# Performance work log

Measured on AMD Instinct MI355X. Metric: run time of the kernel, lower is better.

The kernel has to match this reference:

```python
import jax, jax.numpy as jnp
import numpy as np

N_NODES = 100000
N_EDGES = 1600000
N_FEAT = 512
N_HID = 256
N_CLASS = 40


def setup_inputs() -> dict:
    key = jax.random.key(0)
    ks = jax.random.split(key, 6)
    features = jax.random.normal(ks[0], (N_NODES, N_FEAT), dtype=jnp.float32)
    edge_index = jax.random.randint(ks[1], (2, N_EDGES), 0, N_NODES, dtype=jnp.int32)
    edge_weight = jax.random.uniform(ks[2], (N_EDGES,), dtype=jnp.float32)
    # xavier_uniform with gain=1.414 (as in reset_parameters)
    g = 1.414
    lim1 = g * np.sqrt(6.0 / (N_FEAT + N_HID))
    lim2 = g * np.sqrt(6.0 / (N_HID + N_CLASS))
    W1 = jax.random.uniform(ks[3], (N_FEAT, N_HID), minval=-lim1, maxval=lim1, dtype=jnp.float32)
    W2 = jax.random.uniform(ks[4], (N_HID, N_CLASS), minval=-lim2, maxval=lim2, dtype=jnp.float32)
    b1 = jnp.zeros((N_HID,), dtype=jnp.float32)
    b2 = jnp.zeros((N_CLASS,), dtype=jnp.float32)
    return {"features": features, "edge_index": edge_index, "edge_weight": edge_weight,
            "W1": W1, "b1": b1, "W2": W2, "b2": b2}


def _spmm(edge_index, edge_weight, x, n):
    # out[r] = sum over edges e with row[e]==r of w[e] * x[col[e]]
    row, col = edge_index[0], edge_index[1]
    msgs = edge_weight[:, None] * x[col]  # [E, D]
    return jax.ops.segment_sum(msgs, row, num_segments=n)


def reference(features, edge_index, edge_weight, W1, b1, W2, b2):
    n = features.shape[0]
    # Layer 1: linear -> spmm -> relu (dropout is identity in eval mode)
    h = features @ W1 + b1
    h = jax.nn.relu(_spmm(edge_index, edge_weight, h, n))
    # Layer 2: linear -> spmm -> log_softmax
    h = h @ W2 + b2
    h = _spmm(edge_index, edge_weight, h, n)
    return jax.nn.log_softmax(h, axis=1)
```

## Files before the change

kernel.cpp:

```cpp
#include <hip/hip_runtime.h>
#include <stdint.h>

#define N_NODES 100000
#define N_EDGES 1600000
#define N_FEAT 512
#define N_HID 256
#define N_CLASS 40
#define H2S 48

typedef float f32x4 __attribute__((ext_vector_type(4)));
typedef __bf16 bf16x8 __attribute__((ext_vector_type(8)));
typedef unsigned short u16x4 __attribute__((ext_vector_type(4)));
typedef unsigned short u16x8 __attribute__((ext_vector_type(8)));

__device__ __forceinline__ unsigned short f2bf(float f) {
  unsigned int u = __float_as_uint(f);
  unsigned int r = (u + 0x7FFFu + ((u >> 16) & 1u)) >> 16;
  return (unsigned short)r;
}
__device__ __forceinline__ float bf2f(unsigned short s) {
  return __uint_as_float(((unsigned int)s) << 16);
}

#define HIST_BLOCKS 1563
#define W1T_BLOCKS  512
#define W2T_BLOCKS  48
__global__ __launch_bounds__(256) void k_pre(const float* __restrict__ W1,
                                             const float* __restrict__ W2,
                                             const int* __restrict__ ei,
                                             unsigned short* __restrict__ W1t,
                                             unsigned short* __restrict__ W2t,
                                             int* __restrict__ cnt,
                                             int* __restrict__ rank) {
  const int bid = blockIdx.x, tid = threadIdx.x;
  if (bid < HIST_BLOCKS) {
    #pragma unroll
    for (int k = 0; k < 4; ++k) {
      int e = bid * 1024 + k * 256 + tid;
      if (e < N_EDGES) rank[e] = atomicAdd(&cnt[ei[e]], 1);
    }
  } else if (bid < HIST_BLOCKS + W1T_BLOCKS) {
    int gid = (bid - HIST_BLOCKS) * 256 + tid;
    int n = gid >> 9, k = gid & 511;
    W1t[gid] = f2bf(W1[(long)k * N_HID + n]);
  } else {
    int gid = (bid - HIST_BLOCKS - W1T_BLOCKS) * 256 + tid;
    int n = gid >> 8, k = gid & 255;
    W2t[gid] = (n < N_CLASS) ? f2bf(W2[(long)k * N_CLASS + n]) : (unsigned short)0;
  }
}

__global__ __launch_bounds__(1024) void k_scan_a(const int* __restrict__ cnt,
                                                 int* __restrict__ rp,
                                                 int* __restrict__ bsum) {
  __shared__ int sm[1024];
  const int tid = threadIdx.x;
  const int i = blockIdx.x * 1024 + tid;
  int v = (i < N_NODES) ? cnt[i] : 0;
  sm[tid] = v;
  __syncthreads();
  #pragma unroll
  for (int d = 1; d < 1024; d <<= 1) {
    int t = (tid >= d) ? sm[tid - d] : 0;
    __syncthreads();
    sm[tid] += t;
    __syncthreads();
  }
  if (i < N_NODES) rp[i] = sm[tid] - v;
  if (tid == 1023) bsum[blockIdx.x] = sm[1023];
}

__global__ __launch_bounds__(128) void k_scan_b(const int* __restrict__ bsum,
                                                int* __restrict__ boffs,
                                                int* __restrict__ rp) {
  __shared__ int sm[128];
  const int tid = threadIdx.x;
  const int nb = (N_NODES + 1023) >> 10;
  int v = (tid < nb) ? bsum[tid] : 0;
  sm[tid] = v;
  __syncthreads();
  #pragma unroll
  for (int d = 1; d < 128; d <<= 1) {
    int t = (tid >= d) ? sm[tid - d] : 0;
    __syncthreads();
    sm[tid] += t;
    __syncthreads();
  }
  boffs[tid] = sm[tid] - v;
  if (tid == 127) rp[N_NODES] = sm[127];
}

__global__ void k_scan_c(int* __restrict__ rp, const int* __restrict__ boffs) {
  int i = blockIdx.x * 256 + threadIdx.x;
  if (i >= N_NODES) return;
  rp[i] += boffs[i >> 10];
}

#define NG1 782
__global__ __launch_bounds__(512) void k_fused1(const float* __restrict__ X,
                                                const unsigned short* __restrict__ W1t,
                                                const float* __restrict__ b1,
                                                unsigned short* __restrict__ H1,
                                                const int* __restrict__ ei,
                                                const float* __restrict__ ew,
                                                const int* __restrict__ rank,
                                                const int* __restrict__ rp,
                                                int2* __restrict__ cw) {
  __shared__ unsigned short As[128][40];
  __shared__ unsigned short Bs[256][40];
  const int t = threadIdx.x;

  if (blockIdx.x & 1) {
    int sb = blockIdx.x >> 1;
    #pragma unroll
    for (int k = 0; k < 4; ++k) {
      int e = sb * 2048 + k * 512 + t;
      if (e < N_EDGES) {
        int r = ei[e];
        int pos = rp[r] + rank[e];
        cw[pos] = make_int2(ei[N_EDGES + e], __float_as_int(ew[e]));
      }
    }
    return;
  }

  const int gb = blockIdx.x >> 1;
  const int lane = t & 63;
  const int wid = t >> 6;
  const int wm = wid >> 2, wn = wid & 3;
  const long m0 = (long)gb * 128;

  f32x4 acc[4][4] = {};
  const int ar = t >> 2;
  const int ak = (t & 3) * 8;
  const long arow = m0 + ar;
  const bool avalid = arow < N_NODES;
  const float* xs = X + arow * N_FEAT;
  const unsigned short* ws0 = W1t + (long)ar * N_FEAT;
  const unsigned short* ws1 = W1t + (long)(ar + 128) * N_FEAT;

  f32x4 xa = {}, xb = {};
  if (avalid) { xa = *(const f32x4*)(xs + ak); xb = *(const f32x4*)(xs + ak + 4); }
  u16x8 wa = *(const u16x8*)(ws0 + ak);
  u16x8 wb = *(const u16x8*)(ws1 + ak);

  for (int k0 = 0; k0 < N_FEAT; k0 += 32) {
    __syncthreads();
    u16x8 ap;
    ap[0] = f2bf(xa[0]); ap[1] = f2bf(xa[1]); ap[2] = f2bf(xa[2]); ap[3] = f2bf(xa[3]);
    ap[4] = f2bf(xb[0]); ap[5] = f2bf(xb[1]); ap[6] = f2bf(xb[2]); ap[7] = f2bf(xb[3]);
    *(u16x8*)&As[ar][ak] = ap;
    *(u16x8*)&Bs[ar][ak] = wa;
    *(u16x8*)&Bs[ar + 128][ak] = wb;
    __syncthreads();

    if (k0 + 32 < N_FEAT) {
      int ko = k0 + 32 + ak;
      if (avalid) { xa = *(const f32x4*)(xs + ko); xb = *(const f32x4*)(xs + ko + 4); }
      wa = *(const u16x8*)(ws0 + ko);
      wb = *(const u16x8*)(ws1 + ko);
    }

    bf16x8 a[4], b[4];
    #pragma unroll
    for (int mt = 0; mt < 4; ++mt)
      a[mt] = *(const bf16x8*)&As[wm * 64 + mt * 16 + (lane & 15)][(lane >> 4) * 8];
    #pragma unroll
    for (int nt = 0; nt < 4; ++nt)
      b[nt] = *(const bf16x8*)&Bs[wn * 64 + nt * 16 + (lane & 15)][(lane >> 4) * 8];
    #pragma unroll
    for (int mt = 0; mt < 4; ++mt)
      #pragma unroll
      for (int nt = 0; nt < 4; ++nt)
        acc[mt][nt] = __builtin_amdgcn_mfma_f32_16x16x32_bf16(a[mt], b[nt], acc[mt][nt], 0, 0, 0);
  }

  #pragma unroll
  for (int nt = 0; nt < 4; ++nt) {
    int col = wn * 64 + nt * 16 + (lane & 15);
    float bias = b1[col];
    #pragma unroll
    for (int mt = 0; mt < 4; ++mt) {
      #pragma unroll
      for (int i = 0; i < 4; ++i) {
        long row = m0 + wm * 64 + mt * 16 + (lane >> 4) * 4 + i;
        if (row < N_NODES) H1[row * N_HID + col] = f2bf(acc[mt][nt][i] + bias);
      }
    }
  }
}

__global__ __launch_bounds__(256) void k_spmm1(const int* __restrict__ row_ptr,
                                               const int2* __restrict__ cw,
                                               const unsigned short* __restrict__ H1,
                                               unsigned short* __restrict__ H1r) {
  int r = blockIdx.x * 4 + (threadIdx.x >> 6);
  int lane = threadIdx.x & 63;
  if (r >= N_NODES) return;
  int s = row_ptr[r], e = row_ptr[r + 1];
  float a0 = 0.f, a1 = 0.f, a2 = 0.f, a3 = 0.f;
  const unsigned short* Hb = H1 + lane * 4;
  int i = s;
  for (; i + 8 <= e; i += 8) {
    int2 c0 = cw[i + 0]; int2 c1 = cw[i + 1]; int2 c2 = cw[i + 2]; int2 c3 = cw[i + 3];
    int2 c4 = cw[i + 4]; int2 c5 = cw[i + 5]; int2 c6 = cw[i + 6]; int2 c7 = cw[i + 7];
    u16x4 h0 = *(const u16x4*)(Hb + (long)c0.x * N_HID);
    u16x4 h1 = *(const u16x4*)(Hb + (long)c1.x * N_HID);
    u16x4 h2 = *(const u16x4*)(Hb + (long)c2.x * N_HID);
    u16x4 h3 = *(const u16x4*)(Hb + (long)c3.x * N_HID);
    u16x4 h4 = *(const u16x4*)(Hb + (long)c4.x * N_HID);
    u16x4 h5 = *(const u16x4*)(Hb + (long)c5.x * N_HID);
    u16x4 h6 = *(const u16x4*)(Hb + (long)c6.x * N_HID);
    u16x4 h7 = *(const u16x4*)(Hb + (long)c7.x * N_HID);
    float w0 = __int_as_float(c0.y), w1 = __int_as_float(c1.y);
    float w2 = __int_as_float(c2.y), w3 = __int_as_float(c3.y);
    float w4 = __int_as_float(c4.y), w5 = __int_as_float(c5.y);
    float w6 = __int_as_float(c6.y), w7 = __int_as_float(c7.y);
    a0 += w0 * bf2f(h0[0]); a1 += w0 * bf2f(h0[1]); a2 += w0 * bf2f(h0[2]); a3 += w0 * bf2f(h0[3]);
    a0 += w1 * bf2f(h1[0]); a1 += w1 * bf2f(h1[1]); a2 += w1 * bf2f(h1[2]); a3 += w1 * bf2f(h1[3]);
    a0 += w2 * bf2f(h2[0]); a1 += w2 * bf2f(h2[1]); a2 += w2 * bf2f(h2[2]); a3 += w2 * bf2f(h2[3]);
    a0 += w3 * bf2f(h3[0]); a1 += w3 * bf2f(h3[1]); a2 += w3 * bf2f(h3[2]); a3 += w3 * bf2f(h3[3]);
    a0 += w4 * bf2f(h4[0]); a1 += w4 * bf2f(h4[1]); a2 += w4 * bf2f(h4[2]); a3 += w4 * bf2f(h4[3]);
    a0 += w5 * bf2f(h5[0]); a1 += w5 * bf2f(h5[1]); a2 += w5 * bf2f(h5[2]); a3 += w5 * bf2f(h5[3]);
    a0 += w6 * bf2f(h6[0]); a1 += w6 * bf2f(h6[1]); a2 += w6 * bf2f(h6[2]); a3 += w6 * bf2f(h6[3]);
    a0 += w7 * bf2f(h7[0]); a1 += w7 * bf2f(h7[1]); a2 += w7 * bf2f(h7[2]); a3 += w7 * bf2f(h7[3]);
  }
  for (; i < e; ++i) {
    int2 cwv = cw[i];
    float w = __int_as_float(cwv.y);
    u16x4 hv = *(const u16x4*)(Hb + (long)cwv.x * N_HID);
    a0 += w * bf2f(hv[0]);
    a1 += w * bf2f(hv[1]);
    a2 += w * bf2f(hv[2]);
    a3 += w * bf2f(hv[3]);
  }
  u16x4 o;
  o[0] = f2bf(fmaxf(a0, 0.f));
  o[1] = f2bf(fmaxf(a1, 0.f));
  o[2] = f2bf(fmaxf(a2, 0.f));
  o[3] = f2bf(fmaxf(a3, 0.f));
  *(u16x4*)(H1r + (long)r * N_HID + lane * 4) = o;
}

__global__ __launch_bounds__(256) void k_gemm2(const unsigned short* __restrict__ H1r,
                                               const unsigned short* __restrict__ W2t,
                                               const float* __restrict__ b2,
                                               float* __restrict__ H2) {
  __shared__ unsigned short As[128][40];
  __shared__ unsigned short Bs[48][40];
  const int t = threadIdx.x;
  const int lane = t & 63;
  const int wid = t >> 6;
  const long m0 = (long)blockIdx.x * 128;
  f32x4 acc[2][3] = {};

  for (int k0 = 0; k0 < N_HID; k0 += 32) {
    __syncthreads();
    #pragma unroll
    for (int p = 0; p < 2; ++p) {
      int u = t + p * 256;
      int rr = u >> 2, kk = (u & 3) * 8;
      long gr = m0 + rr;
      u16x8 v = {};
      if (gr < N_NODES) v = *(const u16x8*)(H1r + gr * N_HID + k0 + kk);
      *(u16x8*)&As[rr][kk] = v;
    }
    if (t < 192) {
      int rr = t >> 2, kk = (t & 3) * 8;
      *(u16x8*)&Bs[rr][kk] = *(const u16x8*)(W2t + (long)rr * N_HID + k0 + kk);
    }
    __syncthreads();

    bf16x8 a[2], b[3];
    #pragma unroll
    for (int mt = 0; mt < 2; ++mt)
      a[mt] = *(const bf16x8*)&As[wid * 32 + mt * 16 + (lane & 15)][(lane >> 4) * 8];
    #pragma unroll
    for (int nt = 0; nt < 3; ++nt)
      b[nt] = *(const bf16x8*)&Bs[nt * 16 + (lane & 15)][(lane >> 4) * 8];
    #pragma unroll
    for (int mt = 0; mt < 2; ++mt)
      #pragma unroll
      for (int nt = 0; nt < 3; ++nt)
        acc[mt][nt] = __builtin_amdgcn_mfma_f32_16x16x32_bf16(a[mt], b[nt], acc[mt][nt], 0, 0, 0);
  }

  #pragma unroll
  for (int nt = 0; nt < 3; ++nt) {
    int col = nt * 16 + (lane & 15);
    if (col < N_CLASS) {
      float bias = b2[col];
      #pragma unroll
      for (int mt = 0; mt < 2; ++mt) {
        #pragma unroll
        for (int i = 0; i < 4; ++i) {
          long row = m0 + wid * 32 + mt * 16 + (lane >> 4) * 4 + i;
          if (row < N_NODES) H2[row * H2S + col] = acc[mt][nt][i] + bias;
        }
      }
    }
  }
}

__global__ __launch_bounds__(256) void k_spmm2_lsm(const int* __restrict__ row_ptr,
                                                   const int2* __restrict__ cw,
                                                   const float* __restrict__ H2,
                                                   float* __restrict__ out) {
  int r = blockIdx.x * 4 + (threadIdx.x >> 6);
  int lane = threadIdx.x & 63;
  if (r >= N_NODES) return;
  int s = row_ptr[r], e = row_ptr[r + 1];
  float acc = 0.f;
  const bool act = lane < N_CLASS;
  int i = s;
  for (; i + 4 <= e; i += 4) {
    int2 c0 = cw[i + 0];
    int2 c1 = cw[i + 1];
    int2 c2 = cw[i + 2];
    int2 c3 = cw[i + 3];
    float h0 = 0.f, h1 = 0.f, h2 = 0.f, h3 = 0.f;
    if (act) {
      h0 = H2[(long)c0.x * H2S + lane];
      h1 = H2[(long)c1.x * H2S + lane];
      h2 = H2[(long)c2.x * H2S + lane];
      h3 = H2[(long)c3.x * H2S + lane];
    }
    acc += __int_as_float(c0.y) * h0;
    acc += __int_as_float(c1.y) * h1;
    acc += __int_as_float(c2.y) * h2;
    acc += __int_as_float(c3.y) * h3;
  }
  for (; i < e; ++i) {
    int2 cwv = cw[i];
    if (act) acc += __int_as_float(cwv.y) * H2[(long)cwv.x * H2S + lane];
  }
  float v = act ? acc : -INFINITY;
  float m = v;
  #pragma unroll
  for (int d = 32; d > 0; d >>= 1) m = fmaxf(m, __shfl_xor(m, d));
  float ex = act ? __expf(v - m) : 0.f;
  float ssum = ex;
  #pragma unroll
  for (int d = 32; d > 0; d >>= 1) ssum += __shfl_xor(ssum, d);
  float ls = __logf(ssum);
  if (act) out[(long)r * N_CLASS + lane] = v - m - ls;
}

extern "C" void kernel_launch(void* const* d_in, const int* in_sizes, int n_in,
                              void* d_out, int out_size, void* d_ws, size_t ws_size,
                              hipStream_t stream) {
  (void)in_sizes; (void)n_in; (void)out_size; (void)ws_size;
  const float* X  = (const float*)d_in[0];
  const int*   EI = (const int*)d_in[1];
  const float* EW = (const float*)d_in[2];
  const float* W1 = (const float*)d_in[3];
  const float* b1 = (const float*)d_in[4];
  const float* W2 = (const float*)d_in[5];
  const float* b2 = (const float*)d_in[6];
  float* out = (float*)d_out;

  char* p = (char*)d_ws;
  auto take = [&](size_t bytes) {
    char* r = p;
    p += (bytes + 511) & ~(size_t)511;
    return r;
  };
  unsigned short* W1t   = (unsigned short*)take((size_t)N_HID * N_FEAT * 2);
  unsigned short* W2t   = (unsigned short*)take((size_t)48 * N_HID * 2);
  int*            cnt   = (int*)take((size_t)N_NODES * 4);
  int*            rp    = (int*)take((size_t)(N_NODES + 1) * 4);
  int*            bsum  = (int*)take((size_t)128 * 4);
  int*            boffs = (int*)take((size_t)128 * 4);
  int*            rank  = (int*)take((size_t)N_EDGES * 4);
  int2*           cw    = (int2*)take((size_t)N_EDGES * 8);
  unsigned short* H1    = (unsigned short*)take((size_t)N_NODES * N_HID * 2);
  unsigned short* H1r   = (unsigned short*)take((size_t)N_NODES * N_HID * 2);
  float*          H2    = (float*)take((size_t)N_NODES * H2S * 4);

  const int NB_SCAN = (N_NODES + 1023) / 1024;

  hipMemsetAsync(cnt, 0, (size_t)N_NODES * 4, stream);
  k_pre<<<HIST_BLOCKS + W1T_BLOCKS + W2T_BLOCKS, 256, 0, stream>>>(W1, W2, EI, W1t, W2t, cnt, rank);
  k_scan_a<<<NB_SCAN, 1024, 0, stream>>>(cnt, rp, bsum);
  k_scan_b<<<1, 128, 0, stream>>>(bsum, boffs, rp);
  k_scan_c<<<(N_NODES + 255) / 256, 256, 0, stream>>>(rp, boffs);
  k_fused1<<<2 * NG1, 512, 0, stream>>>(X, W1t, b1, H1, EI, EW, rank, rp, cw);
  k_spmm1<<<(N_NODES + 3) / 4, 256, 0, stream>>>(rp, cw, H1, H1r);
  k_gemm2<<<(N_NODES + 127) / 128, 256, 0, stream>>>(H1r, W2t, b2, H2);
  k_spmm2_lsm<<<(N_NODES + 3) / 4, 256, 0, stream>>>(rp, cw, H2, out);
}
```

Measured before the change: 437.8 us.

## Load MFMA operands directly from global memory, dropping LDS staging in both GEMMs

Both GEMM kernels stop staging tiles through shared memory: each lane loads its MFMA fragments straight from global memory into registers, with a one-step register prefetch in the first GEMM, and all __syncthreads are removed. Out-of-range rows are clamped to the last valid row instead of being zero-filled. The spmm2 loop is also unrolled from 4 to 8 edges to keep more gathers in flight. The cost is that the global load traffic in GEMM1 is no longer shared across warps: each warp re-reads its own A and B fragments, so L2/global traffic and register pressure go up.

```diff
diff --git a/kernel.cpp b/kernel.cpp
--- a/kernel.cpp
+++ b/kernel.cpp
@@ -106,8 +106,6 @@
                                                 const int* __restrict__ rank,
                                                 const int* __restrict__ rp,
                                                 int2* __restrict__ cw) {
-  __shared__ unsigned short As[128][40];
-  __shared__ unsigned short Bs[256][40];
   const int t = threadIdx.x;
 
   if (blockIdx.x & 1) {
@@ -129,55 +127,68 @@
   const int wid = t >> 6;
   const int wm = wid >> 2, wn = wid & 3;
   const long m0 = (long)gb * 128;
+  const int lr = lane & 15;
+  const int lk = (lane >> 4) * 8;
+
+  const float* Ab[4];
+  #pragma unroll
+  for (int mt = 0; mt < 4; ++mt) {
+    long r = m0 + wm * 64 + mt * 16 + lr;
+    if (r >= N_NODES) r = N_NODES - 1;
+    Ab[mt] = X + r * N_FEAT + lk;
+  }
+  const unsigned short* Bb[4];
+  #pragma unroll
+  for (int nt = 0; nt < 4; ++nt)
+    Bb[nt] = W1t + (long)(wn * 64 + nt * 16 + lr) * N_FEAT + lk;
 
   f32x4 acc[4][4] = {};
-  const int ar = t >> 2;
-  const int ak = (t & 3) * 8;
-  const long arow = m0 + ar;
-  const bool avalid = arow < N_NODES;
-  const float* xs = X + arow * N_FEAT;
-  const unsigned short* ws0 = W1t + (long)ar * N_FEAT;
-  const unsigned short* ws1 = W1t + (long)(ar + 128) * N_FEAT;
-
-  f32x4 xa = {}, xb = {};
-  if (avalid) { xa = *(const f32x4*)(xs + ak); xb = *(const f32x4*)(xs + ak + 4); }
-  u16x8 wa = *(const u16x8*)(ws0 + ak);
-  u16x8 wb = *(const u16x8*)(ws1 + ak);
-
+  f32x4 xa[4], xb[4];
+  bf16x8 bv[4];
+  #pragma unroll
+  for (int mt = 0; mt < 4; ++mt) { xa[mt] = *(const f32x4*)(Ab[mt]); xb[mt] = *(const f32x4*)(Ab[mt] + 4); }
+  #pragma unroll
+  for (int nt = 0; nt < 4; ++nt) bv[nt] = *(const bf16x8*)(Bb[nt]);
+
+  #pragma unroll 2
   for (int k0 = 0; k0 < N_FEAT; k0 += 32) {
-    __syncthreads();
-    u16x8 ap;
-    ap[0] = f2bf(xa[0]); ap[1] = f2bf(xa[1]); ap[2] = f2bf(xa[2]); ap[3] = f2bf(xa[3]);
-    ap[4] = f2bf(xb[0]); ap[5] = f2bf(xb[1]); ap[6] = f2bf(xb[2]); ap[7] = f2bf(xb[3]);
-    *(u16x8*)&As[ar][ak] = ap;
-    *(u16x8*)&Bs[ar][ak] = wa;
-    *(u16x8*)&Bs[ar + 128][ak] = wb;
-    __syncthreads();
-
-    if (k0 + 32 < N_FEAT) {
-      int ko = k0 + 32 + ak;
-      if (avalid) { xa = *(const f32x4*)(xs + ko); xb = *(const f32x4*)(xs + ko + 4); }
-      wa = *(const u16x8*)(ws0 + ko);
-      wb = *(const u16x8*)(ws1 + ko);
-    }
-
-    bf16x8 a[4], b[4];
-    #pragma unroll
-    for (int mt = 0; mt < 4; ++mt)
-      a[mt] = *(const bf16x8*)&As[wm * 64 + mt * 16 + (lane & 15)][(lane >> 4) * 8];
-    #pragma unroll
-    for (int nt = 0; nt < 4; ++nt)
-      b[nt] = *(const bf16x8*)&Bs[wn * 64 + nt * 16 + (lane & 15)][(lane >> 4) * 8];
+    const int kn = (k0 + 32) & (N_FEAT - 1);
+    f32x4 nxa[4], nxb[4];
+    bf16x8 nbv[4];
+    #pragma unroll
+    for (int mt = 0; mt < 4; ++mt) {
+      nxa[mt] = *(const f32x4*)(Ab[mt] + kn);
+      nxb[mt] = *(const f32x4*)(Ab[mt] + kn + 4);
+    }
+    #pragma unroll
+    for (int nt = 0; nt < 4; ++nt) nbv[nt] = *(const bf16x8*)(Bb[nt] + kn);
+
+    bf16x8 av[4];
+    #pragma unroll
+    for (int mt = 0; mt < 4; ++mt) {
+      bf16x8 v;
+      v[0] = (__bf16)xa[mt][0]; v[1] = (__bf16)xa[mt][1];
+      v[2] = (__bf16)xa[mt][2]; v[3] = (__bf16)xa[mt][3];
+      v[4] = (__bf16)xb[mt][0]; v[5] = (__bf16)xb[mt][1];
+      v[6] = (__bf16)xb[mt][2]; v[7] = (__bf16)xb[mt][3];
+      av[mt] = v;
+    }
+
     #pragma unroll
     for (int mt = 0; mt < 4; ++mt)
       #pragma unroll
       for (int nt = 0; nt < 4; ++nt)
-        acc[mt][nt] = __builtin_amdgcn_mfma_f32_16x16x32_bf16(a[mt], b[nt], acc[mt][nt], 0, 0, 0);
+        acc[mt][nt] = __builtin_amdgcn_mfma_f32_16x16x32_bf16(av[mt], bv[nt], acc[mt][nt], 0, 0, 0);
+
+    #pragma unroll
+    for (int mt = 0; mt < 4; ++mt) { xa[mt] = nxa[mt]; xb[mt] = nxb[mt]; }
+    #pragma unroll
+    for (int nt = 0; nt < 4; ++nt) bv[nt] = nbv[nt];
   }
 
   #pragma unroll
   for (int nt = 0; nt < 4; ++nt) {
-    int col = wn * 64 + nt * 16 + (lane & 15);
+    int col = wn * 64 + nt * 16 + lr;
     float bias = b1[col];
     #pragma unroll
     for (int mt = 0; mt < 4; ++mt) {
@@ -246,48 +257,43 @@
                                                const unsigned short* __restrict__ W2t,
                                                const float* __restrict__ b2,
                                                float* __restrict__ H2) {
-  __shared__ unsigned short As[128][40];
-  __shared__ unsigned short Bs[48][40];
   const int t = threadIdx.x;
   const int lane = t & 63;
   const int wid = t >> 6;
   const long m0 = (long)blockIdx.x * 128;
+  const int lr = lane & 15;
+  const int lk = (lane >> 4) * 8;
+
+  const unsigned short* Ab[2];
+  #pragma unroll
+  for (int mt = 0; mt < 2; ++mt) {
+    long r = m0 + wid * 32 + mt * 16 + lr;
+    if (r >= N_NODES) r = N_NODES - 1;
+    Ab[mt] = H1r + r * N_HID + lk;
+  }
+  const unsigned short* Bb[3];
+  #pragma unroll
+  for (int nt = 0; nt < 3; ++nt)
+    Bb[nt] = W2t + (long)(nt * 16 + lr) * N_HID + lk;
+
   f32x4 acc[2][3] = {};
-
+  #pragma unroll
   for (int k0 = 0; k0 < N_HID; k0 += 32) {
-    __syncthreads();
-    #pragma unroll
-    for (int p = 0; p < 2; ++p) {
-      int u = t + p * 256;
-      int rr = u >> 2, kk = (u & 3) * 8;
-      long gr = m0 + rr;
-      u16x8 v = {};
-      if (gr < N_NODES) v = *(const u16x8*)(H1r + gr * N_HID + k0 + kk);
-      *(u16x8*)&As[rr][kk] = v;
-    }
-    if (t < 192) {
-      int rr = t >> 2, kk = (t & 3) * 8;
-      *(u16x8*)&Bs[rr][kk] = *(const u16x8*)(W2t + (long)rr * N_HID + k0 + kk);
-    }
-    __syncthreads();
-
-    bf16x8 a[2], b[3];
-    #pragma unroll
-    for (int mt = 0; mt < 2; ++mt)
-      a[mt] = *(const bf16x8*)&As[wid * 32 + mt * 16 + (lane & 15)][(lane >> 4) * 8];
-    #pragma unroll
-    for (int nt = 0; nt < 3; ++nt)
-      b[nt] = *(const bf16x8*)&Bs[nt * 16 + (lane & 15)][(lane >> 4) * 8];
+    bf16x8 av[2], bvv[3];
+    #pragma unroll
+    for (int mt = 0; mt < 2; ++mt) av[mt] = *(const bf16x8*)(Ab[mt] + k0);
+    #pragma unroll
+    for (int nt = 0; nt < 3; ++nt) bvv[nt] = *(const bf16x8*)(Bb[nt] + k0);
     #pragma unroll
     for (int mt = 0; mt < 2; ++mt)
       #pragma unroll
       for (int nt = 0; nt < 3; ++nt)
-        acc[mt][nt] = __builtin_amdgcn_mfma_f32_16x16x32_bf16(a[mt], b[nt], acc[mt][nt], 0, 0, 0);
+        acc[mt][nt] = __builtin_amdgcn_mfma_f32_16x16x32_bf16(av[mt], bvv[nt], acc[mt][nt], 0, 0, 0);
   }
 
   #pragma unroll
   for (int nt = 0; nt < 3; ++nt) {
-    int col = nt * 16 + (lane & 15);
+    int col = nt * 16 + lr;
     if (col < N_CLASS) {
       float bias = b2[col];
       #pragma unroll
@@ -313,22 +319,28 @@
   float acc = 0.f;
   const bool act = lane < N_CLASS;
   int i = s;
-  for (; i + 4 <= e; i += 4) {
-    int2 c0 = cw[i + 0];
-    int2 c1 = cw[i + 1];
-    int2 c2 = cw[i + 2];
-    int2 c3 = cw[i + 3];
-    float h0 = 0.f, h1 = 0.f, h2 = 0.f, h3 = 0.f;
+  for (; i + 8 <= e; i += 8) {
+    int2 c0 = cw[i + 0]; int2 c1 = cw[i + 1]; int2 c2 = cw[i + 2]; int2 c3 = cw[i + 3];
+    int2 c4 = cw[i + 4]; int2 c5 = cw[i + 5]; int2 c6 = cw[i + 6]; int2 c7 = cw[i + 7];
+    float h0 = 0.f, h1 = 0.f, h2 = 0.f, h3 = 0.f, h4 = 0.f, h5 = 0.f, h6 = 0.f, h7 = 0.f;
     if (act) {
       h0 = H2[(long)c0.x * H2S + lane];
       h1 = H2[(long)c1.x * H2S + lane];
       h2 = H2[(long)c2.x * H2S + lane];
       h3 = H2[(long)c3.x * H2S + lane];
+      h4 = H2[(long)c4.x * H2S + lane];
+      h5 = H2[(long)c5.x * H2S + lane];
+      h6 = H2[(long)c6.x * H2S + lane];
+      h7 = H2[(long)c7.x * H2S + lane];
     }
     acc += __int_as_float(c0.y) * h0;
     acc += __int_as_float(c1.y) * h1;
     acc += __int_as_float(c2.y) * h2;
     acc += __int_as_float(c3.y) * h3;
+    acc += __int_as_float(c4.y) * h4;
+    acc += __int_as_float(c5.y) * h5;
+    acc += __int_as_float(c6.y) * h6;
+    acc += __int_as_float(c7.y) * h7;
   }
   for (; i < e; ++i) {
     int2 cwv = cw[i];
```

Result: slower. 670.0 us (+53.0%).
